# Kernel optimization log

Measured on AMD Instinct MI355X. Metric: run time of the kernel, lower is better.

## Reference

```python
import jax, jax.numpy as jnp
import numpy as np

B, S, D = 8, 2048, 768

def setup_inputs() -> dict:
    key = jax.random.key(0)
    kx, kq, kk, kv = jax.random.split(key, 4)
    scale = 1.0 / np.sqrt(D)
    x = jax.random.normal(kx, (B, S, D), dtype=jnp.float32)
    # nn.Linear weights: [out, in], applied as x @ W.T
    Wq = jax.random.normal(kq, (D, D), dtype=jnp.float32) * scale
    Wk = jax.random.normal(kk, (D, D), dtype=jnp.float32) * scale
    Wv = jax.random.normal(kv, (D, D), dtype=jnp.float32) * scale
    return {"x": x, "Wq": Wq, "Wk": Wk, "Wv": Wv}

def reference(x, Wq, Wk, Wv):
    d_k = x.shape[-1]
    Q = jnp.einsum('bsd,ed->bse', x, Wq)
    K = jnp.einsum('bsd,ed->bse', x, Wk)
    V = jnp.einsum('bsd,ed->bse', x, Wv)
    scores = jnp.einsum('bqd,bkd->bqk', Q, K) / jnp.sqrt(jnp.float32(d_k))
    attention_weights = jax.nn.softmax(scores, axis=-1)  # [B,S,S]
    weighted_values = jnp.einsum('bqk,bkd->bqd', attention_weights, V)
    return (weighted_values, attention_weights)
```

## Files before the change

### kernel.cpp

```cpp
#include <hip/hip_runtime.h>
#include <cmath>


typedef __bf16 v8bf __attribute__((ext_vector_type(8)));
typedef float  v4f  __attribute__((ext_vector_type(4)));
typedef unsigned short u16;

__device__ __forceinline__ u16 f2bf(float f) {
  union { float f; unsigned u; } v; v.f = f;
  unsigned r = v.u + 0x7fffu + ((v.u >> 16) & 1u);
  return (u16)(r >> 16);
}

__device__ __forceinline__ uint4 pack8(const float* __restrict__ src) {
  float4 f0 = *(const float4*)src;
  float4 f1 = *(const float4*)(src + 4);
  union { uint4 u; u16 h[8]; } pk;
  pk.h[0] = f2bf(f0.x); pk.h[1] = f2bf(f0.y); pk.h[2] = f2bf(f0.z); pk.h[3] = f2bf(f0.w);
  pk.h[4] = f2bf(f1.x); pk.h[5] = f2bf(f1.y); pk.h[6] = f2bf(f1.z); pk.h[7] = f2bf(f1.w);
  return pk.u;
}

__device__ __forceinline__ void gl_lds16(const void* g, void* l) {
  __builtin_amdgcn_global_load_lds(
      (const __attribute__((address_space(1))) unsigned*)g,
      (__attribute__((address_space(3))) unsigned*)l, 16, 0, 0);
}

enum { OUT_F32 = 0, OUT_QKV = 1 };

constexpr int BM = 128, BN = 128, BK = 64;
constexpr int TILE = BM * BK;

template <bool A_F32, int MODE>
__global__ __launch_bounds__(256)
void gemm128(const void* __restrict__ Ag_, const void* __restrict__ Bg_,
             void* __restrict__ C0, void* __restrict__ C1, void* __restrict__ C2,
             int K, int lda, int ldb, int ldc,
             long long sA, long long sB, long long sC, float alpha) {
  __shared__ u16 As[2 * TILE];
  __shared__ u16 Bs[2 * TILE];

  const int z  = blockIdx.z;
  const int m0 = blockIdx.x * BM;
  const int n0 = blockIdx.y * BN;

  const int t    = threadIdx.x;
  const int lane = t & 63;
  const int w    = t >> 6;
  const int wm   = (w & 1) * 64;
  const int wn   = (w >> 1) * 64;
  const int fr   = lane & 15;
  const int quad = lane >> 4;

  const u16* Bp = (const u16*)Bg_ + (size_t)z * (size_t)sB;

  v4f acc[4][4];
#pragma unroll
  for (int i = 0; i < 4; ++i)
#pragma unroll
    for (int j = 0; j < 4; ++j) acc[i][j] = (v4f){0.f, 0.f, 0.f, 0.f};

  auto stage = [&](int kt, int buf) {
#pragma unroll
    for (int j = 0; j < 4; ++j) {
      const int s   = (w * 4 + j) * 64 + lane;
      const int row = s >> 3;
      const int gc  = (s & 7) ^ (row & 7);
      gl_lds16(Bp + (size_t)(n0 + row) * ldb + kt + gc * 8,
               &Bs[buf * TILE + s * 8]);
    }
    if constexpr (A_F32) {
      const float* Ap = (const float*)Ag_ + (size_t)z * (size_t)sA;
#pragma unroll
      for (int j = 0; j < 4; ++j) {
        const int g   = j * 256 + t;
        const int row = g >> 3, gc = g & 7;
        const int s   = (g & ~7) | (gc ^ (row & 7));
        uint4 pk = pack8(Ap + (size_t)(m0 + row) * lda + kt + gc * 8);
        *(uint4*)&As[buf * TILE + s * 8] = pk;
      }
    } else {
      const u16* Ap = (const u16*)Ag_ + (size_t)z * (size_t)sA;
#pragma unroll
      for (int j = 0; j < 4; ++j) {
        const int s   = (w * 4 + j) * 64 + lane;
        const int row = s >> 3;
        const int gc  = (s & 7) ^ (row & 7);
        gl_lds16(Ap + (size_t)(m0 + row) * lda + kt + gc * 8,
                 &As[buf * TILE + s * 8]);
      }
    }
  };

  stage(0, 0);
  __syncthreads();

  int cur = 0;
  for (int kt = 0; kt < K; kt += BK) {
    if (kt + BK < K) stage(kt + BK, cur ^ 1);

    const u16* Ab = &As[cur * TILE];
    const u16* Bb = &Bs[cur * TILE];
#pragma unroll
    for (int kk = 0; kk < BK; kk += 32) {
      const int kc = (kk >> 3) + quad;
      v8bf af[4], bv[4];
#pragma unroll
      for (int i = 0; i < 4; ++i) {
        const int ra = wm + i * 16 + fr;
        const int rb = wn + i * 16 + fr;
        af[i] = *(const v8bf*)&Ab[(ra * 8 + (kc ^ (fr & 7))) * 8];
        bv[i] = *(const v8bf*)&Bb[(rb * 8 + (kc ^ (fr & 7))) * 8];
      }
#pragma unroll
      for (int mi = 0; mi < 4; ++mi)
#pragma unroll
        for (int ni = 0; ni < 4; ++ni)
          acc[mi][ni] =
              __builtin_amdgcn_mfma_f32_16x16x32_bf16(af[mi], bv[ni], acc[mi][ni], 0, 0, 0);
    }
    __syncthreads();
    cur ^= 1;
  }

  const int r0 = (lane >> 4) * 4;
#pragma unroll
  for (int mi = 0; mi < 4; ++mi) {
#pragma unroll
    for (int ni = 0; ni < 4; ++ni) {
      v4f v = acc[mi][ni];
      const int grow0 = m0 + wm + mi * 16 + r0;
      const int gcol  = n0 + wn + ni * 16 + fr;
      if constexpr (MODE == OUT_F32) {
        float* C = (float*)C0 + (size_t)z * (size_t)sC;
#pragma unroll
        for (int r = 0; r < 4; ++r)
          C[(size_t)(grow0 + r) * ldc + gcol] = v[r] * alpha;
      } else {
        const int grp  = n0 / 768;
        const int lcol = (n0 - grp * 768) + wn + ni * 16 + fr;
        if (grp == 0) {
          u16* C = (u16*)C0;
#pragma unroll
          for (int r = 0; r < 4; ++r)
            C[(size_t)(grow0 + r) * 768 + lcol] = f2bf(v[r]);
        } else if (grp == 1) {
          u16* C = (u16*)C1;
#pragma unroll
          for (int r = 0; r < 4; ++r)
            C[(size_t)(grow0 + r) * 768 + lcol] = f2bf(v[r]);
        } else {
          u16* C = (u16*)C2;
          size_t base = (size_t)(grow0 >> 11) * (768ull * 2048ull) +
                        (size_t)lcol * 2048ull + (size_t)(grow0 & 2047);
          ushort4 st;
          st.x = f2bf(v[0]); st.y = f2bf(v[1]); st.z = f2bf(v[2]); st.w = f2bf(v[3]);
          *(ushort4*)&C[base] = st;
        }
      }
    }
  }
}

__global__ __launch_bounds__(256)
void cvt_bf16(const float* __restrict__ src, u16* __restrict__ dst, int n8) {
  const int i = blockIdx.x * 256 + threadIdx.x;
  if (i < n8) *(uint4*)(dst + (size_t)i * 8) = pack8(src + (size_t)i * 8);
}

__global__ __launch_bounds__(256)
void cvt3_bf16(const float* __restrict__ s0, const float* __restrict__ s1,
               const float* __restrict__ s2, u16* __restrict__ d0,
               u16* __restrict__ d1, u16* __restrict__ d2, int n8) {
  const float* s = blockIdx.y == 0 ? s0 : blockIdx.y == 1 ? s1 : s2;
  u16*         d = blockIdx.y == 0 ? d0 : blockIdx.y == 1 ? d1 : d2;
  const int i = blockIdx.x * 256 + threadIdx.x;
  if (i < n8) *(uint4*)(d + (size_t)i * 8) = pack8(s + (size_t)i * 8);
}

template <bool EMIT>
__global__ __launch_bounds__(256) void softmax_rows(float* __restrict__ w,
                                                    u16* __restrict__ pb) {
  float* p = w + (size_t)blockIdx.x * 2048;
  const int t = threadIdx.x;
  float4 a = *(float4*)(p + t * 4);
  float4 b = *(float4*)(p + 1024 + t * 4);

  float mx = fmaxf(fmaxf(fmaxf(a.x, a.y), fmaxf(a.z, a.w)),
                   fmaxf(fmaxf(b.x, b.y), fmaxf(b.z, b.w)));
#pragma unroll
  for (int off = 32; off; off >>= 1) mx = fmaxf(mx, __shfl_xor(mx, off));
  __shared__ float red[4];
  const int wid = t >> 6, ln = t & 63;
  if (ln == 0) red[wid] = mx;
  __syncthreads();
  mx = fmaxf(fmaxf(red[0], red[1]), fmaxf(red[2], red[3]));

  a.x = __expf(a.x - mx); a.y = __expf(a.y - mx);
  a.z = __expf(a.z - mx); a.w = __expf(a.w - mx);
  b.x = __expf(b.x - mx); b.y = __expf(b.y - mx);
  b.z = __expf(b.z - mx); b.w = __expf(b.w - mx);

  float s = a.x + a.y + a.z + a.w + b.x + b.y + b.z + b.w;
#pragma unroll
  for (int off = 32; off; off >>= 1) s += __shfl_xor(s, off);
  __syncthreads();
  if (ln == 0) red[wid] = s;
  __syncthreads();
  s = red[0] + red[1] + red[2] + red[3];

  const float inv = 1.0f / s;
  a.x *= inv; a.y *= inv; a.z *= inv; a.w *= inv;
  b.x *= inv; b.y *= inv; b.z *= inv; b.w *= inv;
  *(float4*)(p + t * 4) = a;
  *(float4*)(p + 1024 + t * 4) = b;

  if constexpr (EMIT) {
    u16* q = pb + (size_t)blockIdx.x * 2048;
    ushort4 ha, hb;
    ha.x = f2bf(a.x); ha.y = f2bf(a.y); ha.z = f2bf(a.z); ha.w = f2bf(a.w);
    hb.x = f2bf(b.x); hb.y = f2bf(b.y); hb.z = f2bf(b.z); hb.w = f2bf(b.w);
    *(ushort4*)(q + t * 4) = ha;
    *(ushort4*)(q + 1024 + t * 4) = hb;
  }
}

extern "C" void kernel_launch(void* const* d_in, const int* in_sizes, int n_in,
                              void* d_out, int out_size, void* d_ws, size_t ws_size,
                              hipStream_t stream) {
  const float* x  = (const float*)d_in[0];
  const float* Wq = (const float*)d_in[1];
  const float* Wk = (const float*)d_in[2];
  const float* Wv = (const float*)d_in[3];
  float* out = (float*)d_out;
  float* wts = out + 8ull * 2048 * 768;

  u16* Qb  = (u16*)d_out;
  u16* Kb  = Qb + 16384ull * 768;
  u16* xb  = (u16*)wts;
  u16* Wqb = xb + 16384ull * 768;
  u16* Wkb = Wqb + 768ull * 768;
  u16* Wvb = Wkb + 768ull * 768;
  u16* Vt  = (u16*)d_ws;
  u16* Pb  = Vt + 8ull * 768 * 2048;

  const size_t VT_BYTES = 8ull * 768 * 2048 * 2;
  const size_t PB_BYTES = 8ull * 2048 * 2048 * 2;
  const bool   pb_ok    = ws_size >= VT_BYTES + PB_BYTES;

  const dim3 blk(256, 1, 1);
  const float isq = 1.0f / sqrtf(768.0f);

  cvt_bf16<<<dim3(6144, 1, 1), blk, 0, stream>>>(x, xb, 16384 * 768 / 8);
  cvt3_bf16<<<dim3(288, 3, 1), blk, 0, stream>>>(Wq, Wk, Wv, Wqb, Wkb, Wvb,
                                                 768 * 768 / 8);

  gemm128<false, OUT_QKV><<<dim3(128, 18, 1), blk, 0, stream>>>(
      xb, Wqb, (void*)Qb, (void*)Kb, (void*)Vt, 768, 768, 768, 768,
      0, 0, 0, 1.0f);

  gemm128<false, OUT_F32><<<dim3(16, 16, 8), blk, 0, stream>>>(
      Qb, Kb, (void*)wts, nullptr, nullptr, 768, 768, 768, 2048,
      2048ll * 768, 2048ll * 768, 2048ll * 2048, isq);

  if (pb_ok) {
    softmax_rows<true><<<dim3(16384, 1, 1), blk, 0, stream>>>(wts, Pb);
    gemm128<false, OUT_F32><<<dim3(16, 6, 8), blk, 0, stream>>>(
        Pb, Vt, (void*)out, nullptr, nullptr, 2048, 2048, 2048, 768,
        2048ll * 2048, 768ll * 2048, 2048ll * 768, 1.0f);
  } else {
    softmax_rows<false><<<dim3(16384, 1, 1), blk, 0, stream>>>(wts, nullptr);
    gemm128<true, OUT_F32><<<dim3(16, 6, 8), blk, 0, stream>>>(
        wts, Vt, (void*)out, nullptr, nullptr, 2048, 2048, 2048, 768,
        2048ll * 2048, 768ll * 2048, 2048ll * 768, 1.0f);
  }
}
```

Measured before the change: 493.3 us.

## Single-buffer GEMM LDS and remap workgroups across XCDs

Drops the double-buffered LDS staging in favour of a single buffer, loaded and then synchronised before compute each K step. This halves shared memory per block, which may allow more resident workgroups. It also remaps the linear workgroup ID so that consecutive tiles land on the same XCD chiplet, meant to improve L2 reuse of shared A/B panels. The trade-off is that global loads no longer overlap with MFMA compute inside a block, so the code relies on occupancy to hide that latency.

```diff
diff --git a/kernel.cpp b/kernel.cpp
--- a/kernel.cpp
+++ b/kernel.cpp
@@ -30,7 +30,6 @@
 enum { OUT_F32 = 0, OUT_QKV = 1 };
 
 constexpr int BM = 128, BN = 128, BK = 64;
-constexpr int TILE = BM * BK;
 
 template <bool A_F32, int MODE>
 __global__ __launch_bounds__(256)
@@ -38,12 +37,23 @@
              void* __restrict__ C0, void* __restrict__ C1, void* __restrict__ C2,
              int K, int lda, int ldb, int ldc,
              long long sA, long long sB, long long sC, float alpha) {
-  __shared__ u16 As[2 * TILE];
-  __shared__ u16 Bs[2 * TILE];
-
-  const int z  = blockIdx.z;
-  const int m0 = blockIdx.x * BM;
-  const int n0 = blockIdx.y * BN;
+  __shared__ u16 As[BM * BK];
+  __shared__ u16 Bs[BN * BK];
+
+  const int gx = gridDim.x, gy = gridDim.y;
+  const int nwg = gx * gy * gridDim.z;
+  int lid = blockIdx.x + gx * (blockIdx.y + gy * blockIdx.z);
+  if ((nwg & 7) == 0) {
+    const int cpx = nwg >> 3;
+    lid = (lid & 7) * cpx + (lid >> 3);
+  }
+  const int bx  = lid % gx;
+  const int byz = lid / gx;
+  const int by  = byz % gy;
+  const int z   = byz / gy;
+
+  const int m0 = bx * BM;
+  const int n0 = by * BN;
 
   const int t    = threadIdx.x;
   const int lane = t & 63;
@@ -61,14 +71,13 @@
 #pragma unroll
     for (int j = 0; j < 4; ++j) acc[i][j] = (v4f){0.f, 0.f, 0.f, 0.f};
 
-  auto stage = [&](int kt, int buf) {
+  for (int kt = 0; kt < K; kt += BK) {
 #pragma unroll
     for (int j = 0; j < 4; ++j) {
       const int s   = (w * 4 + j) * 64 + lane;
       const int row = s >> 3;
       const int gc  = (s & 7) ^ (row & 7);
-      gl_lds16(Bp + (size_t)(n0 + row) * ldb + kt + gc * 8,
-               &Bs[buf * TILE + s * 8]);
+      gl_lds16(Bp + (size_t)(n0 + row) * ldb + kt + gc * 8, &Bs[s * 8]);
     }
     if constexpr (A_F32) {
       const float* Ap = (const float*)Ag_ + (size_t)z * (size_t)sA;
@@ -78,7 +87,7 @@
         const int row = g >> 3, gc = g & 7;
         const int s   = (g & ~7) | (gc ^ (row & 7));
         uint4 pk = pack8(Ap + (size_t)(m0 + row) * lda + kt + gc * 8);
-        *(uint4*)&As[buf * TILE + s * 8] = pk;
+        *(uint4*)&As[s * 8] = pk;
       }
     } else {
       const u16* Ap = (const u16*)Ag_ + (size_t)z * (size_t)sA;
@@ -87,21 +96,11 @@
         const int s   = (w * 4 + j) * 64 + lane;
         const int row = s >> 3;
         const int gc  = (s & 7) ^ (row & 7);
-        gl_lds16(Ap + (size_t)(m0 + row) * lda + kt + gc * 8,
-                 &As[buf * TILE + s * 8]);
-      }
-    }
-  };
-
-  stage(0, 0);
-  __syncthreads();
-
-  int cur = 0;
-  for (int kt = 0; kt < K; kt += BK) {
-    if (kt + BK < K) stage(kt + BK, cur ^ 1);
-
-    const u16* Ab = &As[cur * TILE];
-    const u16* Bb = &Bs[cur * TILE];
+        gl_lds16(Ap + (size_t)(m0 + row) * lda + kt + gc * 8, &As[s * 8]);
+      }
+    }
+    __syncthreads();
+
 #pragma unroll
     for (int kk = 0; kk < BK; kk += 32) {
       const int kc = (kk >> 3) + quad;
@@ -110,8 +109,8 @@
       for (int i = 0; i < 4; ++i) {
         const int ra = wm + i * 16 + fr;
         const int rb = wn + i * 16 + fr;
-        af[i] = *(const v8bf*)&Ab[(ra * 8 + (kc ^ (fr & 7))) * 8];
-        bv[i] = *(const v8bf*)&Bb[(rb * 8 + (kc ^ (fr & 7))) * 8];
+        af[i] = *(const v8bf*)&As[(ra * 8 + (kc ^ (fr & 7))) * 8];
+        bv[i] = *(const v8bf*)&Bs[(rb * 8 + (kc ^ (fr & 7))) * 8];
       }
 #pragma unroll
       for (int mi = 0; mi < 4; ++mi)
@@ -121,7 +120,6 @@
               __builtin_amdgcn_mfma_f32_16x16x32_bf16(af[mi], bv[ni], acc[mi][ni], 0, 0, 0);
     }
     __syncthreads();
-    cur ^= 1;
   }
 
   const int r0 = (lane >> 4) * 4;
@@ -139,7 +137,7 @@
           C[(size_t)(grow0 + r) * ldc + gcol] = v[r] * alpha;
       } else {
         const int grp  = n0 / 768;
-        const int lcol = (n0 - grp * 768) + wn + ni * 16 + fr;
+        const int lcol = gcol - grp * 768;
         if (grp == 0) {
           u16* C = (u16*)C0;
 #pragma unroll
```

New measurement: 486.0 us. Within noise of the previous version (-1.5%).
